# Optimization experiments

Hardware: AMD Instinct MI355X
Metric: run time of the kernel (lower is better)

The kernel has to match this reference:

```python
import jax, jax.numpy as jnp
import numpy as np

STRIDE, PAD, DIL, DG, GROUPS = 1, 1, 1, 1, 1


def setup_inputs() -> dict:
    key = jax.random.key(0)
    k1, k2, k3, k4 = jax.random.split(key, 4)
    B, Cin, H, W = 4, 64, 128, 128
    Cout, kh, kw = 64, 3, 3
    x = jax.random.normal(k1, (B, Cin, H, W), jnp.float32)
    # learned offsets: [B, dg*2*kh*kw, Ho, Wo], interleaved (y, x) per kernel tap
    offset = jax.random.normal(k2, (B, DG * 2 * kh * kw, H, W), jnp.float32)
    # modulation mask: [B, dg*kh*kw, Ho, Wo] in (0,1) (sigmoid applied upstream in DCNv2 packs)
    mask = jax.random.uniform(k3, (B, DG * kh * kw, H, W), jnp.float32)
    stdv = 1.0 / np.sqrt(Cin * kh * kw)
    weight = jax.random.uniform(k4, (Cout, Cin // GROUPS, kh, kw), jnp.float32, -stdv, stdv)
    bias = jnp.zeros((Cout,), jnp.float32)
    return {"x": x, "offset": offset, "mask": mask, "weight": weight, "bias": bias}


def reference(x, offset, mask, weight, bias):
    B, Cin, H, W = x.shape
    Cout, _, kh, kw = weight.shape
    K2 = kh * kw
    Ho = (H + 2 * PAD - DIL * (kh - 1) - 1) // STRIDE + 1
    Wo = (W + 2 * PAD - DIL * (kw - 1) - 1) // STRIDE + 1
    Cg = Cin // DG

    # base sampling grid per kernel tap: [K2, Ho, Wo]
    ky = (jnp.arange(kh) * DIL).repeat(kw)          # [K2]
    kx = jnp.tile(jnp.arange(kw) * DIL, kh)          # [K2]
    base_y = jnp.arange(Ho) * STRIDE - PAD           # [Ho]
    base_x = jnp.arange(Wo) * STRIDE - PAD           # [Wo]
    grid_y = ky[:, None, None] + base_y[None, :, None]  # [K2, Ho, 1]
    grid_x = kx[:, None, None] + base_x[None, None, :]  # [K2, 1, Wo]

    # offsets: [B, dg, K2, 2, Ho, Wo] with channel 0=y, 1=x (DCNv2 interleaving)
    off = offset.reshape(B, DG, K2, 2, Ho, Wo)
    py = grid_y[None, None].astype(x.dtype) + off[:, :, :, 0]  # [B, dg, K2, Ho, Wo]
    px = grid_x[None, None].astype(x.dtype) + off[:, :, :, 1]

    y0 = jnp.floor(py).astype(jnp.int32)
    x0 = jnp.floor(px).astype(jnp.int32)
    ly = py - y0.astype(x.dtype)
    lx = px - x0.astype(x.dtype)

    xg = x.reshape(B, DG, Cg, H * W)

    def gather(iy, ix):
        valid = ((iy >= 0) & (iy < H) & (ix >= 0) & (ix < W)).astype(x.dtype)
        idx = jnp.clip(iy, 0, H - 1) * W + jnp.clip(ix, 0, W - 1)   # [B, dg, K2, Ho, Wo]
        flat = idx.reshape(B, DG, 1, -1)
        vals = jnp.take_along_axis(xg, flat, axis=3)                 # [B, dg, Cg, K2*Ho*Wo]
        return vals.reshape(B, DG, Cg, K2, Ho, Wo) * valid[:, :, None]

    w00 = ((1 - ly) * (1 - lx))[:, :, None]
    w01 = ((1 - ly) * lx)[:, :, None]
    w10 = (ly * (1 - lx))[:, :, None]
    w11 = (ly * lx)[:, :, None]

    sampled = (gather(y0, x0) * w00 + gather(y0, x0 + 1) * w01
               + gather(y0 + 1, x0) * w10 + gather(y0 + 1, x0 + 1) * w11)
    sampled = sampled * mask.reshape(B, DG, 1, K2, Ho, Wo)

    # im2col GEMM (groups=1): [B, Cin*K2, Ho*Wo] x [Cout, Cin*K2]
    cols = sampled.reshape(B, Cin * K2, Ho * Wo)
    wf = weight.reshape(Cout, Cin * K2)
    out = jnp.einsum('ok,bkp->bop', wf, cols).reshape(B, Cout, Ho, Wo)
    return out + bias[None, :, None, None]
```

## Files before the change

### kernel.cpp

```cpp
#include <hip/hip_runtime.h>
#include <math.h>

#define H_    128
#define W_    128
#define HW_   (H_ * W_)
#define CIN_  64
#define COUT_ 64
#define K2_   9
#define B_    4
#define NROWS 10
#define LDS_BYTES (NROWS * 128 * 128)

typedef __bf16 bf16x8 __attribute__((ext_vector_type(8)));
typedef __bf16 bf16x4 __attribute__((ext_vector_type(4)));
typedef float  f32x4  __attribute__((ext_vector_type(4)));

__global__ __launch_bounds__(256) void wtrans3_kernel(const float* __restrict__ w,
                                                      __bf16* __restrict__ wt3) {
    int idx = blockIdx.x * 256 + threadIdx.x;
    if (idx >= K2_ * 2 * 4 * 64 * 8) return;
    int e    = idx & 7;
    int lane = (idx >> 3) & 63;
    int ct   = (idx >> 9) & 3;
    int s    = (idx >> 11) & 1;
    int k    = idx >> 12;
    int co   = ct * 16 + (lane & 15);
    int cin  = s * 32 + (lane >> 4) * 8 + e;
    wt3[idx] = (__bf16)w[(co * CIN_ + cin) * K2_ + k];
}

__global__ __launch_bounds__(1024, 4) void dcn_lds_kernel(
    const float* __restrict__ x,
    const float* __restrict__ offset,
    const float* __restrict__ mask,
    const __bf16* __restrict__ wt3,
    const float* __restrict__ bias,
    float* __restrict__ out)
{
    extern __shared__ char sm[];

    const int tid  = threadIdx.x;
    const int wave = tid >> 6;
    const int lane = tid & 63;
    const int n16  = lane & 15;
    const int kb   = lane >> 4;

    const int bid0 = blockIdx.x;
    const int bidx = (bid0 & 7) * 32 + (bid0 >> 3);
    const int b   = bidx >> 6;
    const int ho0 = (bidx & 63) * 2;

    const float* xb = x + (size_t)b * CIN_ * HW_;

    {
        const int g5     = tid >> 5;
        const int px4    = tid & 31;
        const int rowpar = g5 >> 4;
        const int c0     = (g5 & 15) * 4;
        const int chunk  = c0 >> 3;
        const int eoff   = (c0 & 7) * 2;
#pragma unroll
        for (int it = 0; it < 5; ++it) {
            const int r = it * 2 + rowpar;
            const int srow = min(max(ho0 - 4 + r, 0), H_ - 1);
            const float* g = xb + ((size_t)c0 * H_ + srow) * W_ + px4 * 4;
            const float4 v0 = *(const float4*)(g);
            const float4 v1 = *(const float4*)(g + HW_);
            const float4 v2 = *(const float4*)(g + 2 * HW_);
            const float4 v3 = *(const float4*)(g + 3 * HW_);
            const float* f0 = (const float*)&v0;
            const float* f1 = (const float*)&v1;
            const float* f2 = (const float*)&v2;
            const float* f3 = (const float*)&v3;
#pragma unroll
            for (int e = 0; e < 4; ++e) {
                const int px = px4 * 4 + e;
                const int q  = (chunk + px + (px >> 3)) & 7;
                bf16x4 pk;
                pk[0] = (__bf16)f0[e];
                pk[1] = (__bf16)f1[e];
                pk[2] = (__bf16)f2[e];
                pk[3] = (__bf16)f3[e];
                *(bf16x4*)(sm + (((size_t)r * 128 + px) * 8 + q) * 16 + eoff) = pk;
            }
        }
    }
    __syncthreads();

    const int rr  = wave >> 3;
    const int til = wave & 7;
    const int ho  = ho0 + rr;
    const int wos = til * 16 + n16;
    const int pix = ho * W_ + wos;
    const float* offb = offset + (size_t)b * (2 * K2_) * HW_ + pix;
    const float* mb   = mask   + (size_t)b * K2_ * HW_ + pix;

    f32x4 acc[4];
#pragma unroll
    for (int t = 0; t < 4; ++t) acc[t] = (f32x4){0.f, 0.f, 0.f, 0.f};

    float oy = offb[0];
    float ox = offb[HW_];
    float mm = mb[0];

#pragma unroll 3
    for (int k = 0; k < K2_; ++k) {
        const int ky = k / 3, kx = k % 3;
        const float py  = (float)(ho - 1 + ky) + oy;
        const float pxf = (float)(wos - 1 + kx) + ox;
        const float fy = floorf(py), fx = floorf(pxf);
        const int   y0 = (int)fy,    x0 = (int)fx;
        const float ly = py - fy,    lx = pxf - fx;

        const float vy0 = (y0 >= 0 && y0 < H_)         ? 1.f : 0.f;
        const float vy1 = (y0 + 1 >= 0 && y0 + 1 < H_) ? 1.f : 0.f;
        const float vx0 = (x0 >= 0 && x0 < W_)         ? 1.f : 0.f;
        const float vx1 = (x0 + 1 >= 0 && x0 + 1 < W_) ? 1.f : 0.f;
        const float W00 = mm * (1.f - ly) * (1.f - lx) * vy0 * vx0;
        const float W01 = mm * (1.f - ly) * lx         * vy0 * vx1;
        const float W10 = mm * ly * (1.f - lx)         * vy1 * vx0;
        const float W11 = mm * ly * lx                 * vy1 * vx1;
        const int cy0 = min(max(y0, 0), H_ - 1);
        const int cy1 = min(max(y0 + 1, 0), H_ - 1);
        const int cx0 = min(max(x0, 0), W_ - 1);
        const int cx1 = min(max(x0 + 1, 0), W_ - 1);

        const int s0 = cy0 - ho0 + 4;
        const int s1 = cy1 - ho0 + 4;
        const bool need0 = ((unsigned)s0 > 9u) && (vy0 != 0.f);
        const bool need1 = ((unsigned)s1 > 9u) && (vy1 != 0.f);
        const int s0c = min(max(s0, 0), 9);
        const int s1c = min(max(s1, 0), 9);
        const int key0 = cx0 + (cx0 >> 3);
        const int key1 = cx1 + (cx1 >> 3);

        const char* r00 = sm + ((size_t)(s0c * 128 + cx0) * 8) * 16;
        const char* r01 = sm + ((size_t)(s0c * 128 + cx1) * 8) * 16;
        const char* r10 = sm + ((size_t)(s1c * 128 + cx0) * 8) * 16;
        const char* r11 = sm + ((size_t)(s1c * 128 + cx1) * 8) * 16;

        bf16x8 a00 = *(const bf16x8*)(r00 + (((kb     + key0) & 7) << 4));
        bf16x8 c00 = *(const bf16x8*)(r00 + (((kb + 4 + key0) & 7) << 4));
        bf16x8 a01 = *(const bf16x8*)(r01 + (((kb     + key1) & 7) << 4));
        bf16x8 c01 = *(const bf16x8*)(r01 + (((kb + 4 + key1) & 7) << 4));
        bf16x8 a10 = *(const bf16x8*)(r10 + (((kb     + key0) & 7) << 4));
        bf16x8 c10 = *(const bf16x8*)(r10 + (((kb + 4 + key0) & 7) << 4));
        bf16x8 a11 = *(const bf16x8*)(r11 + (((kb     + key1) & 7) << 4));
        bf16x8 c11 = *(const bf16x8*)(r11 + (((kb + 4 + key1) & 7) << 4));

        if (__builtin_expect(need0, 0)) {
            const float* gl = xb + (size_t)(kb * 8) * HW_ + (size_t)cy0 * W_;
            const float* gh = gl + (size_t)32 * HW_;
#pragma unroll
            for (int e = 0; e < 8; ++e) {
                a00[e] = (__bf16)gl[(size_t)e * HW_ + cx0];
                a01[e] = (__bf16)gl[(size_t)e * HW_ + cx1];
                c00[e] = (__bf16)gh[(size_t)e * HW_ + cx0];
                c01[e] = (__bf16)gh[(size_t)e * HW_ + cx1];
            }
        }
        if (__builtin_expect(need1, 0)) {
            const float* gl = xb + (size_t)(kb * 8) * HW_ + (size_t)cy1 * W_;
            const float* gh = gl + (size_t)32 * HW_;
#pragma unroll
            for (int e = 0; e < 8; ++e) {
                a10[e] = (__bf16)gl[(size_t)e * HW_ + cx0];
                a11[e] = (__bf16)gl[(size_t)e * HW_ + cx1];
                c10[e] = (__bf16)gh[(size_t)e * HW_ + cx0];
                c11[e] = (__bf16)gh[(size_t)e * HW_ + cx1];
            }
        }

        if (k + 1 < K2_) {
            oy = offb[(2 * (k + 1)) * HW_];
            ox = offb[(2 * (k + 1) + 1) * HW_];
            mm = mb[(k + 1) * HW_];
        }

        bf16x8 bf0, bf1;
#pragma unroll
        for (int e = 0; e < 8; ++e) {
            const float v0 = W00 * (float)a00[e] + W01 * (float)a01[e]
                           + W10 * (float)a10[e] + W11 * (float)a11[e];
            const float v1 = W00 * (float)c00[e] + W01 * (float)c01[e]
                           + W10 * (float)c10[e] + W11 * (float)c11[e];
            bf0[e] = (__bf16)v0;
            bf1[e] = (__bf16)v1;
        }

        const __bf16* wk = wt3 + (size_t)k * (2 * 4 * 64 * 8);
#pragma unroll
        for (int ct = 0; ct < 4; ++ct) {
            const bf16x8 A0 = *(const bf16x8*)(wk + (0 * 4 + ct) * 512 + lane * 8);
            const bf16x8 A1 = *(const bf16x8*)(wk + (1 * 4 + ct) * 512 + lane * 8);
            acc[ct] = __builtin_amdgcn_mfma_f32_16x16x32_bf16(A0, bf0, acc[ct], 0, 0, 0);
            acc[ct] = __builtin_amdgcn_mfma_f32_16x16x32_bf16(A1, bf1, acc[ct], 0, 0, 0);
        }
    }

#pragma unroll
    for (int ct = 0; ct < 4; ++ct) {
#pragma unroll
        for (int r = 0; r < 4; ++r) {
            const int co = ct * 16 + kb * 4 + r;
            out[((size_t)(b * COUT_ + co)) * HW_ + pix] = acc[ct][r] + bias[co];
        }
    }
}

extern "C" void kernel_launch(void* const* d_in, const int* in_sizes, int n_in,
                              void* d_out, int out_size, void* d_ws, size_t ws_size,
                              hipStream_t stream) {
    const float* x      = (const float*)d_in[0];
    const float* offset = (const float*)d_in[1];
    const float* mask   = (const float*)d_in[2];
    const float* weight = (const float*)d_in[3];
    const float* bias   = (const float*)d_in[4];
    float* out = (float*)d_out;
    __bf16* wt3 = (__bf16*)d_ws;

    hipFuncSetAttribute(reinterpret_cast<const void*>(dcn_lds_kernel),
                        hipFuncAttributeMaxDynamicSharedMemorySize, LDS_BYTES);

    wtrans3_kernel<<<(K2_ * 2 * 4 * 64 * 8 + 255) / 256, 256, 0, stream>>>(weight, wt3);
    dcn_lds_kernel<<<B_ * H_ / 2, 1024, LDS_BYTES, stream>>>(x, offset, mask, wt3, bias, out);
}
```

Baseline: 33.13 us.

## Split input channels across two blocks and combine partial outputs with atomics

Each block now handles only half of the 64 input channels for its two output rows, which halves the LDS footprint and doubles the grid size to raise occupancy. Partial results are combined with float atomicAdd into an output buffer zeroed by a memset, and bias is added only by the first half. The cost is a doubled offset/mask load and bilinear-weight computation, atomic traffic on every output, and an extra memset launch.

```diff
diff --git a/kernel.cpp b/kernel.cpp
--- a/kernel.cpp
+++ b/kernel.cpp
@@ -9,7 +9,7 @@
 #define K2_   9
 #define B_    4
 #define NROWS 10
-#define LDS_BYTES (NROWS * 128 * 128)
+#define LDS_BYTES (NROWS * 128 * 64)
 
 typedef __bf16 bf16x8 __attribute__((ext_vector_type(8)));
 typedef __bf16 bf16x4 __attribute__((ext_vector_type(4)));
@@ -29,7 +29,7 @@
     wt3[idx] = (__bf16)w[(co * CIN_ + cin) * K2_ + k];
 }
 
-__global__ __launch_bounds__(1024, 4) void dcn_lds_kernel(
+__global__ __launch_bounds__(1024, 8) void dcn_half_kernel(
     const float* __restrict__ x,
     const float* __restrict__ offset,
     const float* __restrict__ mask,
@@ -46,42 +46,46 @@
     const int kb   = lane >> 4;
 
     const int bid0 = blockIdx.x;
-    const int bidx = (bid0 & 7) * 32 + (bid0 >> 3);
-    const int b   = bidx >> 6;
-    const int ho0 = (bidx & 63) * 2;
-
-    const float* xb = x + (size_t)b * CIN_ * HW_;
+    const int bidx = (bid0 & 7) * 64 + (bid0 >> 3);
+    const int half = bidx >> 8;
+    const int pair = bidx & 255;
+    const int b    = pair >> 6;
+    const int ho0  = (pair & 63) * 2;
+
+    const float* xh = x + (size_t)b * CIN_ * HW_ + (size_t)(half * 32) * HW_;
 
     {
-        const int g5     = tid >> 5;
-        const int px4    = tid & 31;
-        const int rowpar = g5 >> 4;
-        const int c0     = (g5 & 15) * 4;
-        const int chunk  = c0 >> 3;
-        const int eoff   = (c0 & 7) * 2;
-#pragma unroll
-        for (int it = 0; it < 5; ++it) {
-            const int r = it * 2 + rowpar;
-            const int srow = min(max(ho0 - 4 + r, 0), H_ - 1);
-            const float* g = xb + ((size_t)c0 * H_ + srow) * W_ + px4 * 4;
-            const float4 v0 = *(const float4*)(g);
-            const float4 v1 = *(const float4*)(g + HW_);
-            const float4 v2 = *(const float4*)(g + 2 * HW_);
-            const float4 v3 = *(const float4*)(g + 3 * HW_);
-            const float* f0 = (const float*)&v0;
-            const float* f1 = (const float*)&v1;
-            const float* f2 = (const float*)&v2;
-            const float* f3 = (const float*)&v3;
-#pragma unroll
-            for (int e = 0; e < 4; ++e) {
-                const int px = px4 * 4 + e;
-                const int q  = (chunk + px + (px >> 3)) & 7;
-                bf16x4 pk;
-                pk[0] = (__bf16)f0[e];
-                pk[1] = (__bf16)f1[e];
-                pk[2] = (__bf16)f2[e];
-                pk[3] = (__bf16)f3[e];
-                *(bf16x4*)(sm + (((size_t)r * 128 + px) * 8 + q) * 16 + eoff) = pk;
+        const int px4   = tid & 31;
+        const int cg    = (tid >> 5) & 7;
+        const int rowg  = tid >> 8;
+        const int c0    = cg * 4;
+        const int chunk = c0 >> 3;
+        const int eoff  = (c0 & 7) * 2;
+#pragma unroll
+        for (int it = 0; it < 3; ++it) {
+            const int r = it * 4 + rowg;
+            if (r < NROWS) {
+                const int srow = min(max(ho0 - 4 + r, 0), H_ - 1);
+                const float* g = xh + ((size_t)c0 * H_ + srow) * W_ + px4 * 4;
+                const float4 v0 = *(const float4*)(g);
+                const float4 v1 = *(const float4*)(g + HW_);
+                const float4 v2 = *(const float4*)(g + 2 * HW_);
+                const float4 v3 = *(const float4*)(g + 3 * HW_);
+                const float* f0 = (const float*)&v0;
+                const float* f1 = (const float*)&v1;
+                const float* f2 = (const float*)&v2;
+                const float* f3 = (const float*)&v3;
+#pragma unroll
+                for (int e = 0; e < 4; ++e) {
+                    const int px = px4 * 4 + e;
+                    const int q  = (chunk + px + (px >> 3)) & 3;
+                    bf16x4 pk;
+                    pk[0] = (__bf16)f0[e];
+                    pk[1] = (__bf16)f1[e];
+                    pk[2] = (__bf16)f2[e];
+                    pk[3] = (__bf16)f3[e];
+                    *(bf16x4*)(sm + ((size_t)(r * 128 + px)) * 64 + q * 16 + eoff) = pk;
+                }
             }
         }
     }
@@ -112,14 +116,15 @@
         const int   y0 = (int)fy,    x0 = (int)fx;
         const float ly = py - fy,    lx = pxf - fx;
 
-        const float vy0 = (y0 >= 0 && y0 < H_)         ? 1.f : 0.f;
-        const float vy1 = (y0 + 1 >= 0 && y0 + 1 < H_) ? 1.f : 0.f;
+        const float A0 = (y0 >= 0 && y0 < H_)         ? mm * (1.f - ly) : 0.f;
+        const float A1 = (y0 + 1 >= 0 && y0 + 1 < H_) ? mm * ly         : 0.f;
         const float vx0 = (x0 >= 0 && x0 < W_)         ? 1.f : 0.f;
         const float vx1 = (x0 + 1 >= 0 && x0 + 1 < W_) ? 1.f : 0.f;
-        const float W00 = mm * (1.f - ly) * (1.f - lx) * vy0 * vx0;
-        const float W01 = mm * (1.f - ly) * lx         * vy0 * vx1;
-        const float W10 = mm * ly * (1.f - lx)         * vy1 * vx0;
-        const float W11 = mm * ly * lx                 * vy1 * vx1;
+        const float l0x = (1.f - lx) * vx0;
+        const float l1x = lx * vx1;
+        const float W00 = A0 * l0x, W01 = A0 * l1x;
+        const float W10 = A1 * l0x, W11 = A1 * l1x;
+
         const int cy0 = min(max(y0, 0), H_ - 1);
         const int cy1 = min(max(y0 + 1, 0), H_ - 1);
         const int cx0 = min(max(x0, 0), W_ - 1);
@@ -127,47 +132,37 @@
 
         const int s0 = cy0 - ho0 + 4;
         const int s1 = cy1 - ho0 + 4;
-        const bool need0 = ((unsigned)s0 > 9u) && (vy0 != 0.f);
-        const bool need1 = ((unsigned)s1 > 9u) && (vy1 != 0.f);
+        const bool need0 = ((unsigned)s0 > 9u) && (A0 != 0.f);
+        const bool need1 = ((unsigned)s1 > 9u) && (A1 != 0.f);
         const int s0c = min(max(s0, 0), 9);
         const int s1c = min(max(s1, 0), 9);
-        const int key0 = cx0 + (cx0 >> 3);
-        const int key1 = cx1 + (cx1 >> 3);
-
-        const char* r00 = sm + ((size_t)(s0c * 128 + cx0) * 8) * 16;
-        const char* r01 = sm + ((size_t)(s0c * 128 + cx1) * 8) * 16;
-        const char* r10 = sm + ((size_t)(s1c * 128 + cx0) * 8) * 16;
-        const char* r11 = sm + ((size_t)(s1c * 128 + cx1) * 8) * 16;
-
-        bf16x8 a00 = *(const bf16x8*)(r00 + (((kb     + key0) & 7) << 4));
-        bf16x8 c00 = *(const bf16x8*)(r00 + (((kb + 4 + key0) & 7) << 4));
-        bf16x8 a01 = *(const bf16x8*)(r01 + (((kb     + key1) & 7) << 4));
-        bf16x8 c01 = *(const bf16x8*)(r01 + (((kb + 4 + key1) & 7) << 4));
-        bf16x8 a10 = *(const bf16x8*)(r10 + (((kb     + key0) & 7) << 4));
-        bf16x8 c10 = *(const bf16x8*)(r10 + (((kb + 4 + key0) & 7) << 4));
-        bf16x8 a11 = *(const bf16x8*)(r11 + (((kb     + key1) & 7) << 4));
-        bf16x8 c11 = *(const bf16x8*)(r11 + (((kb + 4 + key1) & 7) << 4));
+
+        const int o0 = ((kb + cx0 + (cx0 >> 3)) & 3) << 4;
+        const int o1 = ((kb + cx1 + (cx1 >> 3)) & 3) << 4;
+        const char* r00 = sm + ((size_t)(s0c * 128 + cx0)) * 64;
+        const char* r01 = sm + ((size_t)(s0c * 128 + cx1)) * 64;
+        const char* r10 = sm + ((size_t)(s1c * 128 + cx0)) * 64;
+        const char* r11 = sm + ((size_t)(s1c * 128 + cx1)) * 64;
+
+        bf16x8 a00 = *(const bf16x8*)(r00 + o0);
+        bf16x8 a01 = *(const bf16x8*)(r01 + o1);
+        bf16x8 a10 = *(const bf16x8*)(r10 + o0);
+        bf16x8 a11 = *(const bf16x8*)(r11 + o1);
 
         if (__builtin_expect(need0, 0)) {
-            const float* gl = xb + (size_t)(kb * 8) * HW_ + (size_t)cy0 * W_;
-            const float* gh = gl + (size_t)32 * HW_;
+            const float* gl = xh + (size_t)(kb * 8) * HW_ + (size_t)cy0 * W_;
 #pragma unroll
             for (int e = 0; e < 8; ++e) {
                 a00[e] = (__bf16)gl[(size_t)e * HW_ + cx0];
                 a01[e] = (__bf16)gl[(size_t)e * HW_ + cx1];
-                c00[e] = (__bf16)gh[(size_t)e * HW_ + cx0];
-                c01[e] = (__bf16)gh[(size_t)e * HW_ + cx1];
             }
         }
         if (__builtin_expect(need1, 0)) {
-            const float* gl = xb + (size_t)(kb * 8) * HW_ + (size_t)cy1 * W_;
-            const float* gh = gl + (size_t)32 * HW_;
+            const float* gl = xh + (size_t)(kb * 8) * HW_ + (size_t)cy1 * W_;
 #pragma unroll
             for (int e = 0; e < 8; ++e) {
                 a10[e] = (__bf16)gl[(size_t)e * HW_ + cx0];
                 a11[e] = (__bf16)gl[(size_t)e * HW_ + cx1];
-                c10[e] = (__bf16)gh[(size_t)e * HW_ + cx0];
-                c11[e] = (__bf16)gh[(size_t)e * HW_ + cx1];
             }
         }
 
@@ -177,24 +172,19 @@
             mm = mb[(k + 1) * HW_];
         }
 
-        bf16x8 bf0, bf1;
+        bf16x8 bf0;
 #pragma unroll
         for (int e = 0; e < 8; ++e) {
-            const float v0 = W00 * (float)a00[e] + W01 * (float)a01[e]
-                           + W10 * (float)a10[e] + W11 * (float)a11[e];
-            const float v1 = W00 * (float)c00[e] + W01 * (float)c01[e]
-                           + W10 * (float)c10[e] + W11 * (float)c11[e];
-            bf0[e] = (__bf16)v0;
-            bf1[e] = (__bf16)v1;
-        }
-
-        const __bf16* wk = wt3 + (size_t)k * (2 * 4 * 64 * 8);
+            const float v = W00 * (float)a00[e] + W01 * (float)a01[e]
+                          + W10 * (float)a10[e] + W11 * (float)a11[e];
+            bf0[e] = (__bf16)v;
+        }
+
+        const __bf16* wk = wt3 + (size_t)k * (2 * 4 * 64 * 8) + half * 2048 + lane * 8;
 #pragma unroll
         for (int ct = 0; ct < 4; ++ct) {
-            const bf16x8 A0 = *(const bf16x8*)(wk + (0 * 4 + ct) * 512 + lane * 8);
-            const bf16x8 A1 = *(const bf16x8*)(wk + (1 * 4 + ct) * 512 + lane * 8);
-            acc[ct] = __builtin_amdgcn_mfma_f32_16x16x32_bf16(A0, bf0, acc[ct], 0, 0, 0);
-            acc[ct] = __builtin_amdgcn_mfma_f32_16x16x32_bf16(A1, bf1, acc[ct], 0, 0, 0);
+            const bf16x8 A = *(const bf16x8*)(wk + ct * 512);
+            acc[ct] = __builtin_amdgcn_mfma_f32_16x16x32_bf16(A, bf0, acc[ct], 0, 0, 0);
         }
     }
 
@@ -203,7 +193,8 @@
 #pragma unroll
         for (int r = 0; r < 4; ++r) {
             const int co = ct * 16 + kb * 4 + r;
-            out[((size_t)(b * COUT_ + co)) * HW_ + pix] = acc[ct][r] + bias[co];
+            const float v = acc[ct][r] + (half == 0 ? bias[co] : 0.f);
+            atomicAdd(&out[((size_t)(b * COUT_ + co)) * HW_ + pix], v);
         }
     }
 }
@@ -219,9 +210,11 @@
     float* out = (float*)d_out;
     __bf16* wt3 = (__bf16*)d_ws;
 
-    hipFuncSetAttribute(reinterpret_cast<const void*>(dcn_lds_kernel),
+    hipFuncSetAttribute(reinterpret_cast<const void*>(dcn_half_kernel),
                         hipFuncAttributeMaxDynamicSharedMemorySize, LDS_BYTES);
 
+    hipMemsetAsync(d_out, 0, (size_t)out_size * sizeof(float), stream);
+
     wtrans3_kernel<<<(K2_ * 2 * 4 * 64 * 8 + 255) / 256, 256, 0, stream>>>(weight, wt3);
-    dcn_lds_kernel<<<B_ * H_ / 2, 1024, LDS_BYTES, stream>>>(x, offset, mask, wt3, bias, out);
+    dcn_half_kernel<<<B_ * H_, 1024, LDS_BYTES, stream>>>(x, offset, mask, wt3, bias, out);
 }
```

Result: slower. 61.11 us (+84.5%).
